# Kernel tuning notes

Hardware: AMD Instinct MI355X
Metric: run time of the kernel (lower is better)

## Reference

```python
import jax, jax.numpy as jnp
import numpy as np

GROUP_SIZE = 128
HIDDEN = 2048
INTER = 5632
TOKENS = 8192
_SHIFTS = jnp.arange(8, dtype=jnp.uint32) * 4  # 4-bit nibbles, 8 per int32


def _pack_rows(nib):
    # nib: [in, out] int values in [0,16); pack 8 consecutive rows into one int32
    r, c = nib.shape
    n = nib.reshape(r // 8, 8, c).astype(jnp.uint32)
    packed = jnp.sum(n << _SHIFTS[None, :, None], axis=1, dtype=jnp.uint32)
    return jax.lax.bitcast_convert_type(packed, jnp.int32)  # [in//8, out]


def _pack_cols(nib):
    # nib: [groups, out]; pack 8 consecutive cols into one int32
    g, o = nib.shape
    n = nib.reshape(g, o // 8, 8).astype(jnp.uint32)
    packed = jnp.sum(n << _SHIFTS[None, None, :], axis=-1, dtype=jnp.uint32)
    return jax.lax.bitcast_convert_type(packed, jnp.int32)  # [groups, out//8]


def _dequant(qweight, qzeros, scales, group_size=GROUP_SIZE):
    # GPTQ int4 dequant: w = (q - (z + 1)) * scale, per group of `group_size` input rows
    in_packed, out = qweight.shape
    in_dim = in_packed * 8
    groups = scales.shape[0]
    sh = jnp.arange(8, dtype=jnp.int32) * 4
    q = (qweight[:, None, :] >> sh[None, :, None]) & 0xF       # [in//8, 8, out]
    q = q.reshape(in_dim, out)
    z = (qzeros[:, :, None] >> sh[None, None, :]) & 0xF        # [groups, out//8, 8]
    z = z.reshape(groups, out)
    gidx = jnp.arange(in_dim) // group_size                    # [in]
    w = (q - (z[gidx] + 1)).astype(scales.dtype) * scales[gidx]
    return w  # [in, out]


def setup_inputs() -> dict:
    key = jax.random.key(0)
    ks = jax.random.split(key, 10)
    x = jax.random.normal(ks[0], (TOKENS, HIDDEN), dtype=jnp.float32)

    def make(kq, kz, ksc, in_dim, out_dim):
        qn = jax.random.randint(kq, (in_dim, out_dim), 0, 16, dtype=jnp.int32)
        zn = jax.random.randint(kz, (in_dim // GROUP_SIZE, out_dim), 0, 16, dtype=jnp.int32)
        sc = jax.random.uniform(ksc, (in_dim // GROUP_SIZE, out_dim), jnp.float32, 1e-3, 2e-2)
        return _pack_rows(qn), _pack_cols(zn), sc

    gq, gz, gs = make(ks[1], ks[2], ks[3], HIDDEN, INTER)
    uq, uz, us = make(ks[4], ks[5], ks[6], HIDDEN, INTER)
    dq, dz, ds = make(ks[7], ks[8], ks[9], INTER, HIDDEN)
    return {
        "x": x,
        "gate_qweight": gq, "gate_qzeros": gz, "gate_scales": gs,
        "up_qweight": uq, "up_qzeros": uz, "up_scales": us,
        "down_qweight": dq, "down_qzeros": dz, "down_scales": ds,
    }


def reference(x, gate_qweight, gate_qzeros, gate_scales,
              up_qweight, up_qzeros, up_scales,
              down_qweight, down_qzeros, down_scales):
    wg = _dequant(gate_qweight, gate_qzeros, gate_scales)  # [H, I]
    wu = _dequant(up_qweight, up_qzeros, up_scales)        # [H, I]
    wd = _dequant(down_qweight, down_qzeros, down_scales)  # [I, H]
    # fused_gate_up: silu(x @ Wg) * (x @ Wu)
    h = jax.nn.silu(x @ wg) * (x @ wu)                     # [T, I]
    return h @ wd                                          # [T, H]
```

## Files before the change

kernel.cpp:

```cpp
#include <hip/hip_runtime.h>

#define TOKENS 8192
#define HIDDEN 2048
#define INTER  5632

typedef _Float16 f16x8 __attribute__((ext_vector_type(8)));
typedef float    f32x4 __attribute__((ext_vector_type(4)));

__device__ __forceinline__ void async_copy16(const void* g, void* l) {
  __builtin_amdgcn_global_load_lds(
      (const __attribute__((address_space(1))) unsigned int*)g,
      (__attribute__((address_space(3))) unsigned int*)l, 16, 0, 0);
}

__global__ void k_convert_x(const float* __restrict__ x, _Float16* __restrict__ xs) {
  const int kb = blockIdx.x;
  const int mt = blockIdx.y;
  const int m  = threadIdx.x;
  const float* src = x + (size_t)(mt * 128 + m) * HIDDEN + kb * 8;
  float4 f0 = *(const float4*)src;
  float4 f1 = *(const float4*)(src + 4);
  f16x8 v;
  v[0] = (_Float16)f0.x; v[1] = (_Float16)f0.y; v[2] = (_Float16)f0.z; v[3] = (_Float16)f0.w;
  v[4] = (_Float16)f1.x; v[5] = (_Float16)f1.y; v[6] = (_Float16)f1.z; v[7] = (_Float16)f1.w;
  *(f16x8*)(xs + ((size_t)(mt * 256 + kb) * 128 + m) * 8) = v;
}

__global__ void k_dequant(const unsigned int* __restrict__ qw,
                          const unsigned int* __restrict__ qz,
                          const float* __restrict__ sc,
                          _Float16* __restrict__ out, int N, int N8) {
  const int n  = blockIdx.x * 256 + threadIdx.x;
  const int k8 = blockIdx.y;
  const int g  = k8 >> 4;
  unsigned int q  = qw[(size_t)k8 * N + n];
  unsigned int zw = qz[(size_t)g * N8 + (n >> 3)];
  int   z1 = (int)((zw >> ((n & 7) * 4)) & 0xFu) + 1;
  float s  = sc[(size_t)g * N + n];
  f16x8 w;
#pragma unroll
  for (int j = 0; j < 8; ++j)
    w[j] = (_Float16)((float)((int)((q >> (4 * j)) & 0xFu) - z1) * s);
  *(f16x8*)(out + ((size_t)k8 * N + n) * 8) = w;
}

__global__ __launch_bounds__(256, 2)
void k_gemm_gateup(const _Float16* __restrict__ xs,
                   const _Float16* __restrict__ wg,
                   const _Float16* __restrict__ wu,
                   _Float16* __restrict__ hs) {
  __shared__ _Float16 lds[3 * 8192];
  _Float16* Al  = lds;
  _Float16* Bgl = lds + 8192;
  _Float16* Bul = lds + 16384;
  const int nt = blockIdx.x, mt = blockIdx.y;
  const int tid = threadIdx.x;
  const int wave = tid >> 6, lane = tid & 63;
  const int wm = wave >> 1, wn = wave & 1;
  const int row16 = lane >> 4, col = lane & 15;
  const int slot = wave * 4;

  const _Float16* gA = xs + (size_t)mt * 256 * 1024;

  int afo[4], bfo[4];
#pragma unroll
  for (int i = 0; i < 4; ++i) {
    afo[i] = (row16 * 128 + wm * 64 + i * 16 + col) * 8;
    bfo[i] = (row16 * 128 + wn * 64 + i * 16 + col) * 8;
  }

  const f32x4 zero = {0.f, 0.f, 0.f, 0.f};
  f32x4 accg[4][4], accu[4][4];
#pragma unroll
  for (int i = 0; i < 4; ++i)
#pragma unroll
    for (int j = 0; j < 4; ++j) { accg[i][j] = zero; accu[i][j] = zero; }

  for (int kit = 0; kit < HIDDEN / 64; ++kit) {
    __syncthreads();
#pragma unroll
    for (int q = 0; q < 4; ++q) {
      const int c = (slot + q) * 64 + lane;
      async_copy16(gA + (size_t)kit * 8192 + (size_t)c * 8,
                   (char*)Al + (size_t)(slot + q) * 1024);
      const int kbl = c >> 7, cc = c & 127;
      const size_t bo = ((size_t)(kit * 8 + kbl) * INTER + nt * 128 + cc) * 8;
      async_copy16(wg + bo, (char*)Bgl + (size_t)(slot + q) * 1024);
      async_copy16(wu + bo, (char*)Bul + (size_t)(slot + q) * 1024);
    }
    __syncthreads();
#pragma unroll
    for (int ks = 0; ks < 2; ++ks) {
      const int kadd = ks * 4096;
      f16x8 af[4], bg[4], bu[4];
#pragma unroll
      for (int i = 0; i < 4; ++i) {
        af[i] = *(const f16x8*)(Al  + kadd + afo[i]);
        bg[i] = *(const f16x8*)(Bgl + kadd + bfo[i]);
        bu[i] = *(const f16x8*)(Bul + kadd + bfo[i]);
      }
#pragma unroll
      for (int mi = 0; mi < 4; ++mi)
#pragma unroll
        for (int ni = 0; ni < 4; ++ni) {
          accg[mi][ni] = __builtin_amdgcn_mfma_f32_16x16x32_f16(af[mi], bg[ni], accg[mi][ni], 0, 0, 0);
          accu[mi][ni] = __builtin_amdgcn_mfma_f32_16x16x32_f16(af[mi], bu[ni], accu[mi][ni], 0, 0, 0);
        }
    }
  }
#pragma unroll
  for (int mi = 0; mi < 4; ++mi)
#pragma unroll
    for (int ni = 0; ni < 4; ++ni) {
      const int kg = nt * 128 + wn * 64 + ni * 16 + col;
      const size_t base = (size_t)(mt * (INTER / 8) + (kg >> 3)) * 1024 + (kg & 7);
#pragma unroll
      for (int r = 0; r < 4; ++r) {
        float g = accg[mi][ni][r], u = accu[mi][ni][r];
        float h = g / (1.f + __expf(-g)) * u;
        const int ml = wm * 64 + mi * 16 + row16 * 4 + r;
        hs[base + (size_t)ml * 8] = (_Float16)h;
      }
    }
}

__global__ __launch_bounds__(256, 2)
void k_gemm_down(const _Float16* __restrict__ hs,
                 const _Float16* __restrict__ wd,
                 float* __restrict__ out) {
  __shared__ _Float16 lds[2 * 8192];
  _Float16* Al = lds;
  _Float16* Bl = lds + 8192;
  const int nt = blockIdx.x, mt = blockIdx.y;
  const int tid = threadIdx.x;
  const int wave = tid >> 6, lane = tid & 63;
  const int wm = wave >> 1, wn = wave & 1;
  const int row16 = lane >> 4, col = lane & 15;
  const int slot = wave * 4;

  const _Float16* gA = hs + (size_t)mt * (INTER / 8) * 1024;

  int afo[4], bfo[4];
#pragma unroll
  for (int i = 0; i < 4; ++i) {
    afo[i] = (row16 * 128 + wm * 64 + i * 16 + col) * 8;
    bfo[i] = (row16 * 128 + wn * 64 + i * 16 + col) * 8;
  }

  const f32x4 zero = {0.f, 0.f, 0.f, 0.f};
  f32x4 acc[4][4];
#pragma unroll
  for (int i = 0; i < 4; ++i)
#pragma unroll
    for (int j = 0; j < 4; ++j) acc[i][j] = zero;

  for (int kit = 0; kit < INTER / 64; ++kit) {
    __syncthreads();
#pragma unroll
    for (int q = 0; q < 4; ++q) {
      const int c = (slot + q) * 64 + lane;
      async_copy16(gA + (size_t)kit * 8192 + (size_t)c * 8,
                   (char*)Al + (size_t)(slot + q) * 1024);
      const int kbl = c >> 7, cc = c & 127;
      const size_t bo = ((size_t)(kit * 8 + kbl) * HIDDEN + nt * 128 + cc) * 8;
      async_copy16(wd + bo, (char*)Bl + (size_t)(slot + q) * 1024);
    }
    __syncthreads();
#pragma unroll
    for (int ks = 0; ks < 2; ++ks) {
      const int kadd = ks * 4096;
      f16x8 af[4], bf[4];
#pragma unroll
      for (int i = 0; i < 4; ++i) {
        af[i] = *(const f16x8*)(Al + kadd + afo[i]);
        bf[i] = *(const f16x8*)(Bl + kadd + bfo[i]);
      }
#pragma unroll
      for (int mi = 0; mi < 4; ++mi)
#pragma unroll
        for (int ni = 0; ni < 4; ++ni)
          acc[mi][ni] = __builtin_amdgcn_mfma_f32_16x16x32_f16(af[mi], bf[ni], acc[mi][ni], 0, 0, 0);
    }
  }
#pragma unroll
  for (int mi = 0; mi < 4; ++mi)
#pragma unroll
    for (int ni = 0; ni < 4; ++ni) {
      const int n = nt * 128 + wn * 64 + ni * 16 + col;
#pragma unroll
      for (int r = 0; r < 4; ++r) {
        const int m = mt * 128 + wm * 64 + mi * 16 + row16 * 4 + r;
        out[(size_t)m * HIDDEN + n] = acc[mi][ni][r];
      }
    }
}

extern "C" void kernel_launch(void* const* d_in, const int* in_sizes, int n_in,
                              void* d_out, int out_size, void* d_ws, size_t ws_size,
                              hipStream_t stream) {
  (void)in_sizes; (void)n_in; (void)out_size; (void)ws_size;
  const float*        x  = (const float*)d_in[0];
  const unsigned int* gq = (const unsigned int*)d_in[1];
  const unsigned int* gz = (const unsigned int*)d_in[2];
  const float*        gs = (const float*)d_in[3];
  const unsigned int* uq = (const unsigned int*)d_in[4];
  const unsigned int* uz = (const unsigned int*)d_in[5];
  const float*        us = (const float*)d_in[6];
  const unsigned int* dq = (const unsigned int*)d_in[7];
  const unsigned int* dz = (const unsigned int*)d_in[8];
  const float*        ds = (const float*)d_in[9];
  float* out = (float*)d_out;

  char* ws = (char*)d_ws;
  _Float16* xs  = (_Float16*)ws;
  _Float16* wgd = (_Float16*)(ws + (size_t)TOKENS * HIDDEN * 2);
  _Float16* wud = wgd + (size_t)HIDDEN * INTER;
  _Float16* wdd = wud + (size_t)HIDDEN * INTER;
  _Float16* hs  = wdd + (size_t)INTER * HIDDEN;

  k_convert_x<<<dim3(HIDDEN / 8, TOKENS / 128), 128, 0, stream>>>(x, xs);
  k_dequant<<<dim3(INTER / 256, HIDDEN / 8), 256, 0, stream>>>(gq, gz, gs, wgd, INTER, INTER / 8);
  k_dequant<<<dim3(INTER / 256, HIDDEN / 8), 256, 0, stream>>>(uq, uz, us, wud, INTER, INTER / 8);
  k_dequant<<<dim3(HIDDEN / 256, INTER / 8), 256, 0, stream>>>(dq, dz, ds, wdd, HIDDEN, HIDDEN / 8);
  k_gemm_gateup<<<dim3(INTER / 128, TOKENS / 128), 256, 0, stream>>>(xs, wgd, wud, hs);
  k_gemm_down<<<dim3(HIDDEN / 128, TOKENS / 128), 256, 0, stream>>>(hs, wdd, out);
}
```

Measured before the change: 702.2 us.

## Rewrite GEMMs as 512-thread double-buffered ping-pong pipelines with larger tiles

Both GEMM kernels move to 512-thread workgroups with 128KB of dynamic LDS, double-buffered A/B stages and a fine-grained schedule. That schedule interleaves async global-to-LDS copies with MFMA phases, using explicit barriers, vmcnt waits and setprio. Tiles grow to 256x128 for gate/up and 256x256 for down, and block IDs are remapped so neighbouring blocks share data in cache. The aim is to hide memory latency behind MFMA work and increase operand reuse, at the cost of one workgroup per CU and a fragile hand-scheduled pipeline.

```diff
diff --git a/kernel.cpp b/kernel.cpp
--- a/kernel.cpp
+++ b/kernel.cpp
@@ -12,6 +12,13 @@
       (const __attribute__((address_space(1))) unsigned int*)g,
       (__attribute__((address_space(3))) unsigned int*)l, 16, 0, 0);
 }
+
+#define BAR   __builtin_amdgcn_s_barrier()
+#define SB0   __builtin_amdgcn_sched_barrier(0)
+#define LGKM0 do { asm volatile("s_waitcnt lgkmcnt(0)" ::: "memory"); SB0; } while (0)
+#define WAITVM(n) asm volatile("s_waitcnt vmcnt(" #n ")" ::: "memory")
+#define PRIO(x) __builtin_amdgcn_s_setprio(x)
+
 
 __global__ void k_convert_x(const float* __restrict__ x, _Float16* __restrict__ xs) {
   const int kb = blockIdx.x;
@@ -44,29 +51,33 @@
   *(f16x8*)(out + ((size_t)k8 * N + n) * 8) = w;
 }
 
-__global__ __launch_bounds__(256, 2)
+__global__ __launch_bounds__(512, 1)
 void k_gemm_gateup(const _Float16* __restrict__ xs,
                    const _Float16* __restrict__ wg,
                    const _Float16* __restrict__ wu,
                    _Float16* __restrict__ hs) {
-  __shared__ _Float16 lds[3 * 8192];
-  _Float16* Al  = lds;
-  _Float16* Bgl = lds + 8192;
-  _Float16* Bul = lds + 16384;
-  const int nt = blockIdx.x, mt = blockIdx.y;
-  const int tid = threadIdx.x;
+  extern __shared__ _Float16 lds[];
+  _Float16* A0  = lds;
+  _Float16* A1  = lds + 16384;
+  _Float16* Bg0 = lds + 32768;
+  _Float16* Bg1 = lds + 40960;
+  _Float16* Bu0 = lds + 49152;
+  _Float16* Bu1 = lds + 57344;
+
+  const int bid  = blockIdx.x;
+  const int wgid = (bid & 7) * 176 + (bid >> 3);
+  const int mt = wgid / 44, nt = wgid % 44;
+
+  const int tid  = threadIdx.x;
   const int wave = tid >> 6, lane = tid & 63;
   const int wm = wave >> 1, wn = wave & 1;
   const int row16 = lane >> 4, col = lane & 15;
-  const int slot = wave * 4;
-
-  const _Float16* gA = xs + (size_t)mt * 256 * 1024;
 
   int afo[4], bfo[4];
 #pragma unroll
   for (int i = 0; i < 4; ++i) {
-    afo[i] = (row16 * 128 + wm * 64 + i * 16 + col) * 8;
-    bfo[i] = (row16 * 128 + wn * 64 + i * 16 + col) * 8;
+    afo[i] = (wm >> 1) * 8192 + row16 * 1024 + ((wm & 1) * 64 + i * 16 + col) * 8;
+    bfo[i] = row16 * 1024 + (wn * 64 + i * 16 + col) * 8;
   }
 
   const f32x4 zero = {0.f, 0.f, 0.f, 0.f};
@@ -76,123 +87,195 @@
 #pragma unroll
     for (int j = 0; j < 4; ++j) { accg[i][j] = zero; accu[i][j] = zero; }
 
-  for (int kit = 0; kit < HIDDEN / 64; ++kit) {
-    __syncthreads();
-#pragma unroll
-    for (int q = 0; q < 4; ++q) {
-      const int c = (slot + q) * 64 + lane;
-      async_copy16(gA + (size_t)kit * 8192 + (size_t)c * 8,
-                   (char*)Al + (size_t)(slot + q) * 1024);
-      const int kbl = c >> 7, cc = c & 127;
-      const size_t bo = ((size_t)(kit * 8 + kbl) * INTER + nt * 128 + cc) * 8;
-      async_copy16(wg + bo, (char*)Bgl + (size_t)(slot + q) * 1024);
-      async_copy16(wu + bo, (char*)Bul + (size_t)(slot + q) * 1024);
-    }
-    __syncthreads();
-#pragma unroll
-    for (int ks = 0; ks < 2; ++ks) {
-      const int kadd = ks * 4096;
-      f16x8 af[4], bg[4], bu[4];
-#pragma unroll
-      for (int i = 0; i < 4; ++i) {
-        af[i] = *(const f16x8*)(Al  + kadd + afo[i]);
-        bg[i] = *(const f16x8*)(Bgl + kadd + bfo[i]);
-        bu[i] = *(const f16x8*)(Bul + kadd + bfo[i]);
-      }
-#pragma unroll
-      for (int mi = 0; mi < 4; ++mi)
-#pragma unroll
-        for (int ni = 0; ni < 4; ++ni) {
-          accg[mi][ni] = __builtin_amdgcn_mfma_f32_16x16x32_f16(af[mi], bg[ni], accg[mi][ni], 0, 0, 0);
-          accu[mi][ni] = __builtin_amdgcn_mfma_f32_16x16x32_f16(af[mi], bu[ni], accu[mi][ni], 0, 0, 0);
-        }
-    }
+  f16x8 af[4][2], bf[2][2];
+
+#define GU_LOAD_A(AP) \
+  _Pragma("unroll") for (int mi_ = 0; mi_ < 4; ++mi_) \
+  _Pragma("unroll") for (int ks_ = 0; ks_ < 2; ++ks_) \
+    af[mi_][ks_] = *(const f16x8*)((AP) + afo[mi_] + ks_ * 4096);
+
+#define GU_LOAD_B(BP, nh) \
+  _Pragma("unroll") for (int ni_ = 0; ni_ < 2; ++ni_) \
+  _Pragma("unroll") for (int ks_ = 0; ks_ < 2; ++ks_) \
+    bf[ni_][ks_] = *(const f16x8*)((BP) + bfo[(nh) * 2 + ni_] + ks_ * 4096);
+
+#define GU_MFMA(ACC, nh) \
+  _Pragma("unroll") for (int mi_ = 0; mi_ < 4; ++mi_) \
+  _Pragma("unroll") for (int ni_ = 0; ni_ < 2; ++ni_) \
+  _Pragma("unroll") for (int ks_ = 0; ks_ < 2; ++ks_) \
+    ACC[mi_][(nh) * 2 + ni_] = __builtin_amdgcn_mfma_f32_16x16x32_f16( \
+        af[mi_][ks_], bf[ni_][ks_], ACC[mi_][(nh) * 2 + ni_], 0, 0, 0);
+
+#define GU_STAGE_A(AP, kt) do { const int kt_ = (kt); \
+  _Pragma("unroll") for (int q_ = 0; q_ < 4; ++q_) { \
+    const int i_ = q_ * 512 + tid; \
+    async_copy16(xs + (size_t)(((2 * mt + (i_ >> 10)) * 256 + kt_ * 8 + ((i_ >> 7) & 7)) * 128 + (i_ & 127)) * 8, \
+                 (char*)(AP) + q_ * 8192 + wave * 1024); } } while (0)
+
+#define GU_STAGE_B(BP, W, kt) do { const int kt_ = (kt); \
+  _Pragma("unroll") for (int q_ = 0; q_ < 2; ++q_) { \
+    const int i_ = q_ * 512 + tid; \
+    async_copy16((W) + (size_t)((kt_ * 8 + (i_ >> 7)) * INTER + nt * 128 + (i_ & 127)) * 8, \
+                 (char*)(BP) + q_ * 8192 + wave * 1024); } } while (0)
+
+  GU_STAGE_A(A0, 0); GU_STAGE_B(Bg0, wg, 0); GU_STAGE_B(Bu0, wu, 0);
+  GU_STAGE_A(A1, 1); GU_STAGE_B(Bg1, wg, 1);
+  WAITVM(6);
+  BAR; SB0;
+
+  for (int t2 = 0; t2 < 16; ++t2) {
+    const int O  = 2 * t2 + 1;
+    const int e2 = (2 * t2 + 2 < 32) ? 2 * t2 + 2 : 31;
+    const int o2 = (2 * t2 + 3 < 32) ? 2 * t2 + 3 : 31;
+    GU_LOAD_A(A0); GU_LOAD_B(Bg0, 0); GU_STAGE_B(Bu1, wu, O);
+    BAR; LGKM0; PRIO(1); GU_MFMA(accg, 0); PRIO(0); BAR; SB0;
+    GU_LOAD_B(Bg0, 1); GU_STAGE_A(A0, e2);
+    BAR; LGKM0; PRIO(1); GU_MFMA(accg, 1); PRIO(0); BAR; SB0;
+    GU_LOAD_B(Bu0, 0); GU_STAGE_B(Bg0, wg, e2);
+    BAR; LGKM0; PRIO(1); GU_MFMA(accu, 0); PRIO(0); BAR; SB0;
+    GU_LOAD_B(Bu0, 1);
+    BAR; LGKM0; PRIO(1); GU_MFMA(accu, 1); PRIO(0); WAITVM(6); BAR; SB0;
+    GU_LOAD_A(A1); GU_LOAD_B(Bg1, 0); GU_STAGE_B(Bu0, wu, e2);
+    BAR; LGKM0; PRIO(1); GU_MFMA(accg, 0); PRIO(0); BAR; SB0;
+    GU_LOAD_B(Bg1, 1); GU_STAGE_A(A1, o2);
+    BAR; LGKM0; PRIO(1); GU_MFMA(accg, 1); PRIO(0); BAR; SB0;
+    GU_LOAD_B(Bu1, 0); GU_STAGE_B(Bg1, wg, o2);
+    BAR; LGKM0; PRIO(1); GU_MFMA(accu, 0); PRIO(0); BAR; SB0;
+    GU_LOAD_B(Bu1, 1);
+    BAR; LGKM0; PRIO(1); GU_MFMA(accu, 1); PRIO(0); WAITVM(6); BAR; SB0;
   }
+  WAITVM(0);
+
+  const size_t mt128 = (size_t)(2 * mt + (wm >> 1));
 #pragma unroll
   for (int mi = 0; mi < 4; ++mi)
 #pragma unroll
     for (int ni = 0; ni < 4; ++ni) {
       const int kg = nt * 128 + wn * 64 + ni * 16 + col;
-      const size_t base = (size_t)(mt * (INTER / 8) + (kg >> 3)) * 1024 + (kg & 7);
+      const size_t base = (mt128 * 704 + (size_t)(kg >> 3)) * 1024 + (kg & 7);
 #pragma unroll
       for (int r = 0; r < 4; ++r) {
-        float g = accg[mi][ni][r], u = accu[mi][ni][r];
-        float h = g / (1.f + __expf(-g)) * u;
-        const int ml = wm * 64 + mi * 16 + row16 * 4 + r;
-        hs[base + (size_t)ml * 8] = (_Float16)h;
+        const float g = accg[mi][ni][r], u = accu[mi][ni][r];
+        const float h = g / (1.f + __expf(-g)) * u;
+        const int mloc = (wm & 1) * 64 + mi * 16 + row16 * 4 + r;
+        hs[base + (size_t)mloc * 8] = (_Float16)h;
       }
     }
-}
-
-__global__ __launch_bounds__(256, 2)
+#undef GU_LOAD_A
+#undef GU_LOAD_B
+#undef GU_MFMA
+#undef GU_STAGE_A
+#undef GU_STAGE_B
+}
+
+__global__ __launch_bounds__(512, 1)
 void k_gemm_down(const _Float16* __restrict__ hs,
                  const _Float16* __restrict__ wd,
                  float* __restrict__ out) {
-  __shared__ _Float16 lds[2 * 8192];
-  _Float16* Al = lds;
-  _Float16* Bl = lds + 8192;
-  const int nt = blockIdx.x, mt = blockIdx.y;
-  const int tid = threadIdx.x;
+  extern __shared__ _Float16 lds[];
+  _Float16* A0 = lds;
+  _Float16* A1 = lds + 16384;
+  _Float16* B0 = lds + 32768;
+  _Float16* B1 = lds + 49152;
+
+  const int bid  = blockIdx.x;
+  const int wgid = (bid & 7) * 32 + (bid >> 3);
+  const int nt = wgid >> 5, mt = wgid & 31;
+
+  const int tid  = threadIdx.x;
   const int wave = tid >> 6, lane = tid & 63;
-  const int wm = wave >> 1, wn = wave & 1;
+  const int wm = wave >> 2, wn = wave & 3;
   const int row16 = lane >> 4, col = lane & 15;
-  const int slot = wave * 4;
-
-  const _Float16* gA = hs + (size_t)mt * (INTER / 8) * 1024;
-
-  int afo[4], bfo[4];
-#pragma unroll
-  for (int i = 0; i < 4; ++i) {
-    afo[i] = (row16 * 128 + wm * 64 + i * 16 + col) * 8;
-    bfo[i] = (row16 * 128 + wn * 64 + i * 16 + col) * 8;
+
+  int afo[8], bfo[4];
+#pragma unroll
+  for (int i = 0; i < 8; ++i)
+    afo[i] = wm * 8192 + row16 * 1024 + (i * 16 + col) * 8;
+#pragma unroll
+  for (int i = 0; i < 4; ++i)
+    bfo[i] = row16 * 2048 + (wn * 64 + i * 16 + col) * 8;
+
+  const f32x4 zero = {0.f, 0.f, 0.f, 0.f};
+  f32x4 acc[8][4];
+#pragma unroll
+  for (int i = 0; i < 8; ++i)
+#pragma unroll
+    for (int j = 0; j < 4; ++j) acc[i][j] = zero;
+
+  f16x8 af[4][2], bf[4][2];
+
+#define DN_LOAD_A(AP, mh) \
+  _Pragma("unroll") for (int mi_ = 0; mi_ < 4; ++mi_) \
+  _Pragma("unroll") for (int ks_ = 0; ks_ < 2; ++ks_) \
+    af[mi_][ks_] = *(const f16x8*)((AP) + afo[(mh) * 4 + mi_] + ks_ * 4096);
+
+#define DN_LOAD_B(BP, nh) \
+  _Pragma("unroll") for (int ni_ = 0; ni_ < 2; ++ni_) \
+  _Pragma("unroll") for (int ks_ = 0; ks_ < 2; ++ks_) \
+    bf[(nh) * 2 + ni_][ks_] = *(const f16x8*)((BP) + bfo[(nh) * 2 + ni_] + ks_ * 8192);
+
+#define DN_MFMA(mh, nh) \
+  _Pragma("unroll") for (int mi_ = 0; mi_ < 4; ++mi_) \
+  _Pragma("unroll") for (int ni_ = 0; ni_ < 2; ++ni_) \
+  _Pragma("unroll") for (int ks_ = 0; ks_ < 2; ++ks_) \
+    acc[(mh) * 4 + mi_][(nh) * 2 + ni_] = __builtin_amdgcn_mfma_f32_16x16x32_f16( \
+        af[mi_][ks_], bf[(nh) * 2 + ni_][ks_], acc[(mh) * 4 + mi_][(nh) * 2 + ni_], 0, 0, 0);
+
+#define DN_STAGE_A(AP, kt) do { const int kt_ = (kt); \
+  _Pragma("unroll") for (int q_ = 0; q_ < 4; ++q_) { \
+    const int i_ = q_ * 512 + tid; \
+    async_copy16(hs + (size_t)(((2 * mt + (i_ >> 10)) * 704 + kt_ * 8 + ((i_ >> 7) & 7)) * 128 + (i_ & 127)) * 8, \
+                 (char*)(AP) + q_ * 8192 + wave * 1024); } } while (0)
+
+#define DN_STAGE_B(BP, kt) do { const int kt_ = (kt); \
+  _Pragma("unroll") for (int q_ = 0; q_ < 4; ++q_) { \
+    const int i_ = q_ * 512 + tid; \
+    async_copy16(wd + (size_t)((kt_ * 8 + (i_ >> 8)) * HIDDEN + nt * 256 + (i_ & 255)) * 8, \
+                 (char*)(BP) + q_ * 8192 + wave * 1024); } } while (0)
+
+  DN_STAGE_B(B0, 0); DN_STAGE_A(A0, 0);
+  DN_STAGE_B(B1, 1); DN_STAGE_A(A1, 1);
+  WAITVM(8);
+  BAR; SB0;
+
+  for (int t2 = 0; t2 < 44; ++t2) {
+    const int e2 = (2 * t2 + 2 < 88) ? 2 * t2 + 2 : 87;
+    const int o2 = (2 * t2 + 3 < 88) ? 2 * t2 + 3 : 87;
+    DN_LOAD_A(A0, 0); DN_LOAD_B(B0, 0);
+    BAR; LGKM0; PRIO(1); DN_MFMA(0, 0); PRIO(0); BAR; SB0;
+    DN_LOAD_B(B0, 1);
+    BAR; LGKM0; PRIO(1); DN_MFMA(0, 1); PRIO(0); BAR; SB0;
+    DN_LOAD_A(A0, 1); DN_STAGE_B(B0, e2);
+    BAR; LGKM0; PRIO(1); DN_MFMA(1, 0); PRIO(0); BAR; SB0;
+    DN_STAGE_A(A0, e2);
+    BAR; LGKM0; PRIO(1); DN_MFMA(1, 1); PRIO(0); WAITVM(8); BAR; SB0;
+    DN_LOAD_A(A1, 0); DN_LOAD_B(B1, 0);
+    BAR; LGKM0; PRIO(1); DN_MFMA(0, 0); PRIO(0); BAR; SB0;
+    DN_LOAD_B(B1, 1);
+    BAR; LGKM0; PRIO(1); DN_MFMA(0, 1); PRIO(0); BAR; SB0;
+    DN_LOAD_A(A1, 1); DN_STAGE_B(B1, o2);
+    BAR; LGKM0; PRIO(1); DN_MFMA(1, 0); PRIO(0); BAR; SB0;
+    DN_STAGE_A(A1, o2);
+    BAR; LGKM0; PRIO(1); DN_MFMA(1, 1); PRIO(0); WAITVM(8); BAR; SB0;
   }
-
-  const f32x4 zero = {0.f, 0.f, 0.f, 0.f};
-  f32x4 acc[4][4];
-#pragma unroll
-  for (int i = 0; i < 4; ++i)
-#pragma unroll
-    for (int j = 0; j < 4; ++j) acc[i][j] = zero;
-
-  for (int kit = 0; kit < INTER / 64; ++kit) {
-    __syncthreads();
-#pragma unroll
-    for (int q = 0; q < 4; ++q) {
-      const int c = (slot + q) * 64 + lane;
-      async_copy16(gA + (size_t)kit * 8192 + (size_t)c * 8,
-                   (char*)Al + (size_t)(slot + q) * 1024);
-      const int kbl = c >> 7, cc = c & 127;
-      const size_t bo = ((size_t)(kit * 8 + kbl) * HIDDEN + nt * 128 + cc) * 8;
-      async_copy16(wd + bo, (char*)Bl + (size_t)(slot + q) * 1024);
-    }
-    __syncthreads();
-#pragma unroll
-    for (int ks = 0; ks < 2; ++ks) {
-      const int kadd = ks * 4096;
-      f16x8 af[4], bf[4];
-#pragma unroll
-      for (int i = 0; i < 4; ++i) {
-        af[i] = *(const f16x8*)(Al + kadd + afo[i]);
-        bf[i] = *(const f16x8*)(Bl + kadd + bfo[i]);
-      }
-#pragma unroll
-      for (int mi = 0; mi < 4; ++mi)
-#pragma unroll
-        for (int ni = 0; ni < 4; ++ni)
-          acc[mi][ni] = __builtin_amdgcn_mfma_f32_16x16x32_f16(af[mi], bf[ni], acc[mi][ni], 0, 0, 0);
-    }
-  }
-#pragma unroll
-  for (int mi = 0; mi < 4; ++mi)
+  WAITVM(0);
+
+#pragma unroll
+  for (int mi = 0; mi < 8; ++mi)
 #pragma unroll
     for (int ni = 0; ni < 4; ++ni) {
-      const int n = nt * 128 + wn * 64 + ni * 16 + col;
+      const int n = nt * 256 + wn * 64 + ni * 16 + col;
 #pragma unroll
       for (int r = 0; r < 4; ++r) {
-        const int m = mt * 128 + wm * 64 + mi * 16 + row16 * 4 + r;
+        const int m = mt * 256 + wm * 128 + mi * 16 + row16 * 4 + r;
         out[(size_t)m * HIDDEN + n] = acc[mi][ni][r];
       }
     }
+#undef DN_LOAD_A
+#undef DN_LOAD_B
+#undef DN_MFMA
+#undef DN_STAGE_A
+#undef DN_STAGE_B
 }
 
 extern "C" void kernel_launch(void* const* d_in, const int* in_sizes, int n_in,
@@ -218,10 +301,19 @@
   _Float16* wdd = wud + (size_t)HIDDEN * INTER;
   _Float16* hs  = wdd + (size_t)INTER * HIDDEN;
 
+  static bool attr_set = false;
+  if (!attr_set) {
+    hipFuncSetAttribute((const void*)k_gemm_gateup,
+                        hipFuncAttributeMaxDynamicSharedMemorySize, 131072);
+    hipFuncSetAttribute((const void*)k_gemm_down,
+                        hipFuncAttributeMaxDynamicSharedMemorySize, 131072);
+    attr_set = true;
+  }
+
   k_convert_x<<<dim3(HIDDEN / 8, TOKENS / 128), 128, 0, stream>>>(x, xs);
   k_dequant<<<dim3(INTER / 256, HIDDEN / 8), 256, 0, stream>>>(gq, gz, gs, wgd, INTER, INTER / 8);
   k_dequant<<<dim3(INTER / 256, HIDDEN / 8), 256, 0, stream>>>(uq, uz, us, wud, INTER, INTER / 8);
   k_dequant<<<dim3(HIDDEN / 256, INTER / 8), 256, 0, stream>>>(dq, dz, ds, wdd, HIDDEN, HIDDEN / 8);
-  k_gemm_gateup<<<dim3(INTER / 128, TOKENS / 128), 256, 0, stream>>>(xs, wgd, wud, hs);
-  k_gemm_down<<<dim3(HIDDEN / 128, TOKENS / 128), 256, 0, stream>>>(hs, wdd, out);
-}
+  k_gemm_gateup<<<dim3(1408), 512, 131072, stream>>>(xs, wgd, wud, hs);
+  k_gemm_down<<<dim3(256), 512, 131072, stream>>>(hs, wdd, out);
+}
```

After: 708.7 us. Within noise of the previous version (+0.9%).

## Rewrite down GEMM as 256x256 double-buffered ping-pong kernel; transpose x conversion via LDS

Applied to the files above, without the earlier changes.

The down-projection GEMM moves to 256x256 tiles with 512 threads, double-buffered LDS (128KB dynamic), staged async copies overlapped with MFMA phases, barrier/priority interleaving, and a swizzled block order for L2 reuse. Separately, the x fp32-to-fp16 conversion now coalesces reads through an LDS transpose. The aim is to hide global-load latency and raise arithmetic intensity in the down GEMM. The cost is a single wave-group per CU and a more fragile hand-scheduled loop.

```diff
diff --git a/kernel.cpp b/kernel.cpp
--- a/kernel.cpp
+++ b/kernel.cpp
@@ -13,17 +13,44 @@
       (__attribute__((address_space(3))) unsigned int*)l, 16, 0, 0);
 }
 
-__global__ void k_convert_x(const float* __restrict__ x, _Float16* __restrict__ xs) {
-  const int kb = blockIdx.x;
-  const int mt = blockIdx.y;
-  const int m  = threadIdx.x;
-  const float* src = x + (size_t)(mt * 128 + m) * HIDDEN + kb * 8;
-  float4 f0 = *(const float4*)src;
-  float4 f1 = *(const float4*)(src + 4);
+#define BAR   __builtin_amdgcn_s_barrier()
+#define SB0   __builtin_amdgcn_sched_barrier(0)
+#define LGKM0 do { asm volatile("s_waitcnt lgkmcnt(0)" ::: "memory"); SB0; } while (0)
+#define WAITVM(n) asm volatile("s_waitcnt vmcnt(" #n ")" ::: "memory")
+#define PRIO(x) __builtin_amdgcn_s_setprio(x)
+
+
+__global__ __launch_bounds__(256)
+void k_convert_x(const float* __restrict__ x, _Float16* __restrict__ xs) {
+  __shared__ float lt[64 * 33];
+  const int kb0  = blockIdx.x;
+  const int mt32 = blockIdx.y;
+  const int t    = threadIdx.x;
+
+  const int m_l  = t >> 3;
+  const int k4a  = t & 7;
+  const float* row = x + (size_t)(mt32 * 32 + m_l) * HIDDEN + kb0 * 64;
+#pragma unroll
+  for (int h = 0; h < 2; ++h) {
+    const int k4 = k4a + h * 8;
+    const float4 f = *(const float4*)(row + k4 * 4);
+    lt[(k4 * 4 + 0) * 33 + m_l] = f.x;
+    lt[(k4 * 4 + 1) * 33 + m_l] = f.y;
+    lt[(k4 * 4 + 2) * 33 + m_l] = f.z;
+    lt[(k4 * 4 + 3) * 33 + m_l] = f.w;
+  }
+  __syncthreads();
+
+  const int kb_l = t >> 5;
+  const int m_o  = t & 31;
   f16x8 v;
-  v[0] = (_Float16)f0.x; v[1] = (_Float16)f0.y; v[2] = (_Float16)f0.z; v[3] = (_Float16)f0.w;
-  v[4] = (_Float16)f1.x; v[5] = (_Float16)f1.y; v[6] = (_Float16)f1.z; v[7] = (_Float16)f1.w;
-  *(f16x8*)(xs + ((size_t)(mt * 256 + kb) * 128 + m) * 8) = v;
+#pragma unroll
+  for (int j = 0; j < 8; ++j)
+    v[j] = (_Float16)lt[(kb_l * 8 + j) * 33 + m_o];
+  const int kb   = kb0 * 8 + kb_l;
+  const int mt128 = mt32 >> 2;
+  const int m128  = (mt32 & 3) * 32 + m_o;
+  *(f16x8*)(xs + ((size_t)(mt128 * 256 + kb) * 128 + m128) * 8) = v;
 }
 
 __global__ void k_dequant(const unsigned int* __restrict__ qw,
@@ -124,75 +151,114 @@
     }
 }
 
-__global__ __launch_bounds__(256, 2)
+__global__ __launch_bounds__(512, 1)
 void k_gemm_down(const _Float16* __restrict__ hs,
                  const _Float16* __restrict__ wd,
                  float* __restrict__ out) {
-  __shared__ _Float16 lds[2 * 8192];
-  _Float16* Al = lds;
-  _Float16* Bl = lds + 8192;
-  const int nt = blockIdx.x, mt = blockIdx.y;
-  const int tid = threadIdx.x;
+  extern __shared__ _Float16 lds[];
+  _Float16* A0 = lds;
+  _Float16* A1 = lds + 16384;
+  _Float16* B0 = lds + 32768;
+  _Float16* B1 = lds + 49152;
+
+  const int bid  = blockIdx.x;
+  const int wgid = (bid & 7) * 32 + (bid >> 3);
+  const int nt = wgid >> 5, mt = wgid & 31;
+
+  const int tid  = threadIdx.x;
   const int wave = tid >> 6, lane = tid & 63;
-  const int wm = wave >> 1, wn = wave & 1;
+  const int wm = wave >> 2, wn = wave & 3;
   const int row16 = lane >> 4, col = lane & 15;
-  const int slot = wave * 4;
-
-  const _Float16* gA = hs + (size_t)mt * (INTER / 8) * 1024;
-
-  int afo[4], bfo[4];
-#pragma unroll
-  for (int i = 0; i < 4; ++i) {
-    afo[i] = (row16 * 128 + wm * 64 + i * 16 + col) * 8;
-    bfo[i] = (row16 * 128 + wn * 64 + i * 16 + col) * 8;
-  }
+
+  int afo[8], bfo[4];
+#pragma unroll
+  for (int i = 0; i < 8; ++i)
+    afo[i] = wm * 8192 + row16 * 1024 + (i * 16 + col) * 8;
+#pragma unroll
+  for (int i = 0; i < 4; ++i)
+    bfo[i] = row16 * 2048 + (wn * 64 + i * 16 + col) * 8;
 
   const f32x4 zero = {0.f, 0.f, 0.f, 0.f};
-  f32x4 acc[4][4];
-#pragma unroll
-  for (int i = 0; i < 4; ++i)
+  f32x4 acc[8][4];
+#pragma unroll
+  for (int i = 0; i < 8; ++i)
 #pragma unroll
     for (int j = 0; j < 4; ++j) acc[i][j] = zero;
 
-  for (int kit = 0; kit < INTER / 64; ++kit) {
-    __syncthreads();
-#pragma unroll
-    for (int q = 0; q < 4; ++q) {
-      const int c = (slot + q) * 64 + lane;
-      async_copy16(gA + (size_t)kit * 8192 + (size_t)c * 8,
-                   (char*)Al + (size_t)(slot + q) * 1024);
-      const int kbl = c >> 7, cc = c & 127;
-      const size_t bo = ((size_t)(kit * 8 + kbl) * HIDDEN + nt * 128 + cc) * 8;
-      async_copy16(wd + bo, (char*)Bl + (size_t)(slot + q) * 1024);
-    }
-    __syncthreads();
-#pragma unroll
-    for (int ks = 0; ks < 2; ++ks) {
-      const int kadd = ks * 4096;
-      f16x8 af[4], bf[4];
-#pragma unroll
-      for (int i = 0; i < 4; ++i) {
-        af[i] = *(const f16x8*)(Al + kadd + afo[i]);
-        bf[i] = *(const f16x8*)(Bl + kadd + bfo[i]);
-      }
-#pragma unroll
-      for (int mi = 0; mi < 4; ++mi)
-#pragma unroll
-        for (int ni = 0; ni < 4; ++ni)
-          acc[mi][ni] = __builtin_amdgcn_mfma_f32_16x16x32_f16(af[mi], bf[ni], acc[mi][ni], 0, 0, 0);
-    }
-  }
-#pragma unroll
-  for (int mi = 0; mi < 4; ++mi)
+  f16x8 af[4][2], bf[4][2];
+
+#define DN_LOAD_A(AP, mh) \
+  _Pragma("unroll") for (int mi_ = 0; mi_ < 4; ++mi_) \
+  _Pragma("unroll") for (int ks_ = 0; ks_ < 2; ++ks_) \
+    af[mi_][ks_] = *(const f16x8*)((AP) + afo[(mh) * 4 + mi_] + ks_ * 4096);
+
+#define DN_LOAD_B(BP, nh) \
+  _Pragma("unroll") for (int ni_ = 0; ni_ < 2; ++ni_) \
+  _Pragma("unroll") for (int ks_ = 0; ks_ < 2; ++ks_) \
+    bf[(nh) * 2 + ni_][ks_] = *(const f16x8*)((BP) + bfo[(nh) * 2 + ni_] + ks_ * 8192);
+
+#define DN_MFMA(mh, nh) \
+  _Pragma("unroll") for (int mi_ = 0; mi_ < 4; ++mi_) \
+  _Pragma("unroll") for (int ni_ = 0; ni_ < 2; ++ni_) \
+  _Pragma("unroll") for (int ks_ = 0; ks_ < 2; ++ks_) \
+    acc[(mh) * 4 + mi_][(nh) * 2 + ni_] = __builtin_amdgcn_mfma_f32_16x16x32_f16( \
+        af[mi_][ks_], bf[(nh) * 2 + ni_][ks_], acc[(mh) * 4 + mi_][(nh) * 2 + ni_], 0, 0, 0);
+
+#define DN_STAGE_A(AP, kt) do { const int kt_ = (kt); \
+  _Pragma("unroll") for (int q_ = 0; q_ < 4; ++q_) { \
+    const int i_ = q_ * 512 + tid; \
+    async_copy16(hs + (size_t)(((2 * mt + (i_ >> 10)) * 704 + kt_ * 8 + ((i_ >> 7) & 7)) * 128 + (i_ & 127)) * 8, \
+                 (char*)(AP) + q_ * 8192 + wave * 1024); } } while (0)
+
+#define DN_STAGE_B(BP, kt) do { const int kt_ = (kt); \
+  _Pragma("unroll") for (int q_ = 0; q_ < 4; ++q_) { \
+    const int i_ = q_ * 512 + tid; \
+    async_copy16(wd + (size_t)((kt_ * 8 + (i_ >> 8)) * HIDDEN + nt * 256 + (i_ & 255)) * 8, \
+                 (char*)(BP) + q_ * 8192 + wave * 1024); } } while (0)
+
+  DN_STAGE_B(B0, 0); DN_STAGE_A(A0, 0);
+  DN_STAGE_B(B1, 1); DN_STAGE_A(A1, 1);
+  WAITVM(8);
+  BAR; SB0;
+
+  for (int t2 = 0; t2 < 44; ++t2) {
+    const int e2 = (2 * t2 + 2 < 88) ? 2 * t2 + 2 : 87;
+    const int o2 = (2 * t2 + 3 < 88) ? 2 * t2 + 3 : 87;
+    DN_LOAD_A(A0, 0); DN_LOAD_B(B0, 0);
+    BAR; LGKM0; PRIO(1); DN_MFMA(0, 0); PRIO(0); BAR; SB0;
+    DN_LOAD_B(B0, 1);
+    BAR; LGKM0; PRIO(1); DN_MFMA(0, 1); PRIO(0); BAR; SB0;
+    DN_LOAD_A(A0, 1); DN_STAGE_B(B0, e2);
+    BAR; LGKM0; PRIO(1); DN_MFMA(1, 0); PRIO(0); BAR; SB0;
+    DN_STAGE_A(A0, e2);
+    BAR; LGKM0; PRIO(1); DN_MFMA(1, 1); PRIO(0); WAITVM(8); BAR; SB0;
+    DN_LOAD_A(A1, 0); DN_LOAD_B(B1, 0);
+    BAR; LGKM0; PRIO(1); DN_MFMA(0, 0); PRIO(0); BAR; SB0;
+    DN_LOAD_B(B1, 1);
+    BAR; LGKM0; PRIO(1); DN_MFMA(0, 1); PRIO(0); BAR; SB0;
+    DN_LOAD_A(A1, 1); DN_STAGE_B(B1, o2);
+    BAR; LGKM0; PRIO(1); DN_MFMA(1, 0); PRIO(0); BAR; SB0;
+    DN_STAGE_A(A1, o2);
+    BAR; LGKM0; PRIO(1); DN_MFMA(1, 1); PRIO(0); WAITVM(8); BAR; SB0;
+  }
+  WAITVM(0);
+
+#pragma unroll
+  for (int mi = 0; mi < 8; ++mi)
 #pragma unroll
     for (int ni = 0; ni < 4; ++ni) {
-      const int n = nt * 128 + wn * 64 + ni * 16 + col;
+      const int n = nt * 256 + wn * 64 + ni * 16 + col;
 #pragma unroll
       for (int r = 0; r < 4; ++r) {
-        const int m = mt * 128 + wm * 64 + mi * 16 + row16 * 4 + r;
+        const int m = mt * 256 + wm * 128 + mi * 16 + row16 * 4 + r;
         out[(size_t)m * HIDDEN + n] = acc[mi][ni][r];
       }
     }
+#undef DN_LOAD_A
+#undef DN_LOAD_B
+#undef DN_MFMA
+#undef DN_STAGE_A
+#undef DN_STAGE_B
 }
 
 extern "C" void kernel_launch(void* const* d_in, const int* in_sizes, int n_in,
@@ -218,10 +284,17 @@
   _Float16* wdd = wud + (size_t)HIDDEN * INTER;
   _Float16* hs  = wdd + (size_t)INTER * HIDDEN;
 
-  k_convert_x<<<dim3(HIDDEN / 8, TOKENS / 128), 128, 0, stream>>>(x, xs);
+  static bool attr_set = false;
+  if (!attr_set) {
+    hipFuncSetAttribute((const void*)k_gemm_down,
+                        hipFuncAttributeMaxDynamicSharedMemorySize, 131072);
+    attr_set = true;
+  }
+
+  k_convert_x<<<dim3(HIDDEN / 64, TOKENS / 32), 256, 0, stream>>>(x, xs);
   k_dequant<<<dim3(INTER / 256, HIDDEN / 8), 256, 0, stream>>>(gq, gz, gs, wgd, INTER, INTER / 8);
   k_dequant<<<dim3(INTER / 256, HIDDEN / 8), 256, 0, stream>>>(uq, uz, us, wud, INTER, INTER / 8);
   k_dequant<<<dim3(HIDDEN / 256, INTER / 8), 256, 0, stream>>>(dq, dz, ds, wdd, HIDDEN, HIDDEN / 8);
   k_gemm_gateup<<<dim3(INTER / 128, TOKENS / 128), 256, 0, stream>>>(xs, wgd, wud, hs);
-  k_gemm_down<<<dim3(HIDDEN / 128, TOKENS / 128), 256, 0, stream>>>(hs, wdd, out);
-}
+  k_gemm_down<<<dim3(256), 512, 131072, stream>>>(hs, wdd, out);
+}
```

Measured after the change: 661.3 us. 1.06x faster.
